# Kernel optimization log

Measured on AMD Instinct MI355X. Metric: run time of the kernel, lower is better.

Reference implementation:

```python
import jax, jax.numpy as jnp
import numpy as np

D_MODEL = 1024
D_FF = 2048
N_EXPERTS = 4
TOP_K = 2
INIT_STD = 0.02


def setup_inputs() -> dict:
    key = jax.random.key(0)
    ks = jax.random.split(key, 5)
    hidden_states = jax.random.normal(ks[0], (2, 2048, D_MODEL), dtype=jnp.float32)
    # gate: nn.Linear(d_model, num_experts, bias=False) -> weight [E, D]
    w_gate = jax.random.normal(ks[1], (N_EXPERTS, D_MODEL), dtype=jnp.float32) * INIT_STD
    # per-expert GLU MLP weights, stacked over the expert axis
    w_gate_proj = jax.random.normal(ks[2], (N_EXPERTS, D_MODEL, D_FF), dtype=jnp.float32) * INIT_STD
    w_up_proj = jax.random.normal(ks[3], (N_EXPERTS, D_MODEL, D_FF), dtype=jnp.float32) * INIT_STD
    w_down_proj = jax.random.normal(ks[4], (N_EXPERTS, D_FF, D_MODEL), dtype=jnp.float32) * INIT_STD
    return {
        "hidden_states": hidden_states,
        "w_gate": w_gate,
        "w_gate_proj": w_gate_proj,
        "w_up_proj": w_up_proj,
        "w_down_proj": w_down_proj,
    }


def reference(hidden_states, w_gate, w_gate_proj, w_up_proj, w_down_proj):
    B, S, D = hidden_states.shape
    x = hidden_states.reshape(-1, D)  # [T, D]
    # --- routing ---
    router_logits = x @ w_gate.T  # [T, E]
    routing_probs = jax.nn.softmax(router_logits.astype(jnp.float32), axis=-1)
    topw, sel = jax.lax.top_k(routing_probs, TOP_K)  # [T, K]
    topw = topw / jnp.sum(topw, axis=-1, keepdims=True)  # norm_topk_prob=True
    topw = topw.astype(x.dtype)
    # combine weights per (token, expert): zero for non-selected experts
    cw = jnp.sum(jax.nn.one_hot(sel, N_EXPERTS, dtype=x.dtype) * topw[..., None], axis=1)  # [T, E]
    # --- expert GLU MLPs (dense over experts, masked combine) ---
    g = jnp.einsum('td,edf->etf', x, w_gate_proj)  # [E, T, F]
    u = jnp.einsum('td,edf->etf', x, w_up_proj)
    h = jax.nn.gelu(g, approximate=False) * u  # torch F.gelu default = exact erf
    y = jnp.einsum('etf,efd->etd', h, w_down_proj)  # [E, T, D]
    out = jnp.einsum('etd,te->td', y, cw)  # weighted scatter-combine
    # dropout p=0.0 (eval) -> identity
    return out.reshape(B, S, D)
```

## Files before the change

kernel.cpp:

```cpp
#include <hip/hip_runtime.h>
#include <hip/hip_bf16.h>
#include <math.h>


typedef float  f32x4 __attribute__((ext_vector_type(4)));
typedef short  s16x8 __attribute__((ext_vector_type(8)));

__device__ __forceinline__ unsigned short f2bf(float f) {
  union { float f; unsigned int u; } v; v.f = f;
  return (unsigned short)((v.u + 0x7fffu + ((v.u >> 16) & 1u)) >> 16);
}

__device__ __forceinline__ void glds16(const void* g, void* l) {
  __builtin_amdgcn_global_load_lds(
      (const __attribute__((address_space(1))) void*)g,
      (__attribute__((address_space(3))) void*)l, 16, 0, 0);
}

__global__ void k_routing(const float* __restrict__ x, const float* __restrict__ wg,
                          float* __restrict__ cw, int* __restrict__ idx,
                          int* __restrict__ cnt) {
  const int lane = threadIdx.x & 63;
  const int tok  = blockIdx.x * 4 + (threadIdx.x >> 6);
  const float* xr = x + (size_t)tok * 1024;
  float a0 = 0.f, a1 = 0.f, a2 = 0.f, a3 = 0.f;
#pragma unroll
  for (int j = 0; j < 16; ++j) {
    const int d = j * 64 + lane;
    const float xv = xr[d];
    a0 += xv * wg[0 * 1024 + d];
    a1 += xv * wg[1 * 1024 + d];
    a2 += xv * wg[2 * 1024 + d];
    a3 += xv * wg[3 * 1024 + d];
  }
#pragma unroll
  for (int off = 32; off; off >>= 1) {
    a0 += __shfl_xor(a0, off);
    a1 += __shfl_xor(a1, off);
    a2 += __shfl_xor(a2, off);
    a3 += __shfl_xor(a3, off);
  }
  if (lane == 0) {
    float l[4] = {a0, a1, a2, a3};
    const float m = fmaxf(fmaxf(l[0], l[1]), fmaxf(l[2], l[3]));
    float p[4];
#pragma unroll
    for (int e = 0; e < 4; ++e) p[e] = expf(l[e] - m);
    int i1 = 0; float b1 = p[0];
#pragma unroll
    for (int e = 1; e < 4; ++e) if (p[e] > b1) { b1 = p[e]; i1 = e; }
    int i2 = -1; float b2 = -1.f;
#pragma unroll
    for (int e = 0; e < 4; ++e) if (e != i1 && p[e] > b2) { b2 = p[e]; i2 = e; }
    const float inv = 1.f / (b1 + b2);
    float o[4] = {0.f, 0.f, 0.f, 0.f};
    o[i1] = b1 * inv; o[i2] = b2 * inv;
    *(float4*)(cw + (size_t)tok * 4) = make_float4(o[0], o[1], o[2], o[3]);
    const int p1 = atomicAdd(&cnt[i1], 1); idx[i1 * 4096 + p1] = tok;
    const int p2 = atomicAdd(&cnt[i2], 1); idx[i2 * 4096 + p2] = tok;
  }
}

__global__ void k_offsets(const int* __restrict__ cnt, int* __restrict__ off) {
  if (threadIdx.x == 0 && blockIdx.x == 0) {
    int o = 0;
#pragma unroll
    for (int e = 0; e < 4; ++e) { off[e] = o; o += (cnt[e] + 127) & ~127; }
  }
}

__global__ void k_cvt_x(const float* __restrict__ in, unsigned short* __restrict__ out) {
  const int i = blockIdx.x * blockDim.x + threadIdx.x;
  const float4 v = ((const float4*)in)[i];
  ushort4 o;
  o.x = f2bf(v.x); o.y = f2bf(v.y); o.z = f2bf(v.z); o.w = f2bf(v.w);
  ((ushort4*)out)[i] = o;
}

__global__ void k_tcvt_all(const float* __restrict__ wgp, const float* __restrict__ wup,
                           const float* __restrict__ wdp,
                           unsigned short* __restrict__ Wgt, unsigned short* __restrict__ Wut,
                           unsigned short* __restrict__ Wdt) {
  __shared__ float t[32][33];
  const int z = blockIdx.z;
  const float* in; unsigned short* out; int R, C, c0, r0;
  if (z < 8) {
    R = 1024; C = 2048;
    const int e = z & 3;
    in  = (z < 4 ? wgp : wup) + (size_t)e * 1024 * 2048;
    out = (z < 4 ? Wgt : Wut) + (size_t)e * 1024 * 2048;
    c0 = blockIdx.x * 32; r0 = blockIdx.y * 32;
  } else {
    R = 2048; C = 1024;
    const int e = z & 3;
    in  = wdp + (size_t)e * 2048 * 1024;
    out = Wdt + (size_t)e * 2048 * 1024;
    c0 = blockIdx.y * 32; r0 = blockIdx.x * 32;
  }
  const int tx = threadIdx.x, ty = threadIdx.y;
#pragma unroll
  for (int i = 0; i < 4; ++i)
    t[ty + 8 * i][tx] = in[(size_t)(r0 + ty + 8 * i) * C + c0 + tx];
  __syncthreads();
#pragma unroll
  for (int i = 0; i < 4; ++i)
    out[(size_t)(c0 + ty + 8 * i) * R + r0 + tx] = f2bf(t[tx][ty + 8 * i]);
}

__global__ __launch_bounds__(256, 2)
void k_gemm1(const unsigned short* __restrict__ Xb,
             const unsigned short* __restrict__ Wgt,
             const unsigned short* __restrict__ Wut,
             unsigned short* __restrict__ H,
             const int* __restrict__ idx, const int* __restrict__ cnt,
             const int* __restrict__ off) {
  const int w  = (blockIdx.x & 7) * 134 + (blockIdx.x >> 3);
  const int bn = w / 67, mt = w % 67;
  const int o1 = off[1] >> 7, o2 = off[2] >> 7, o3 = off[3] >> 7;
  if (mt >= o3 + ((cnt[3] + 127) >> 7)) return;
  const int e  = (mt >= o1) + (mt >= o2) + (mt >= o3);
  const int ob = (e == 0) ? 0 : (e == 1 ? o1 : (e == 2 ? o2 : o3));
  const int cn = cnt[e];
  const int lr0 = (mt - ob) * 128;

  __shared__ __align__(16) unsigned short sA[128 * 64];
  __shared__ __align__(16) unsigned short sG[128 * 64];
  __shared__ __align__(16) unsigned short sU[128 * 64];
  const int tid = threadIdx.x;
  const int lane = tid & 63, wid = tid >> 6;
  const int wm = wid >> 1, wn = wid & 1;

  f32x4 accg[4][4] = {};
  f32x4 accu[4][4] = {};

  const int srow = lane >> 3;
  const int scol = (lane & 7) * 8;
  int tk[4];
#pragma unroll
  for (int i = 0; i < 4; ++i) {
    const int row = (wid * 4 + i) * 8 + srow;
    tk[i] = idx[e * 4096 + min(lr0 + row, cn - 1)];
  }
  const unsigned short* Wg = Wgt + (size_t)e * 2048 * 1024 + (size_t)(bn * 128) * 1024;
  const unsigned short* Wu = Wut + (size_t)e * 2048 * 1024 + (size_t)(bn * 128) * 1024;

  for (int kt = 0; kt < 16; ++kt) {
    const int k0 = kt * 64;
#pragma unroll
    for (int i = 0; i < 4; ++i) {
      const int c = wid * 4 + i;
      const int row = c * 8 + srow;
      glds16(Xb + (size_t)tk[i] * 1024 + k0 + scol, &sA[c * 512]);
      glds16(Wg + (size_t)row * 1024 + k0 + scol, &sG[c * 512]);
      glds16(Wu + (size_t)row * 1024 + k0 + scol, &sU[c * 512]);
    }
    __syncthreads();
#pragma unroll
    for (int ks = 0; ks < 2; ++ks) {
      const int ko = ks * 32 + (lane >> 4) * 8;
      s16x8 a[4], bg[4], bu[4];
#pragma unroll
      for (int mi = 0; mi < 4; ++mi)
        a[mi] = *(const s16x8*)&sA[(wm * 64 + mi * 16 + (lane & 15)) * 64 + ko];
#pragma unroll
      for (int ni = 0; ni < 4; ++ni) {
        bg[ni] = *(const s16x8*)&sG[(wn * 64 + ni * 16 + (lane & 15)) * 64 + ko];
        bu[ni] = *(const s16x8*)&sU[(wn * 64 + ni * 16 + (lane & 15)) * 64 + ko];
      }
#pragma unroll
      for (int mi = 0; mi < 4; ++mi)
#pragma unroll
        for (int ni = 0; ni < 4; ++ni) {
          accg[mi][ni] = __builtin_amdgcn_mfma_f32_16x16x32_bf16(a[mi], bg[ni], accg[mi][ni], 0, 0, 0);
          accu[mi][ni] = __builtin_amdgcn_mfma_f32_16x16x32_bf16(a[mi], bu[ni], accu[mi][ni], 0, 0, 0);
        }
    }
    __syncthreads();
  }
  const int r0 = mt * 128 + wm * 64;
  const int c0 = bn * 128 + wn * 64;
#pragma unroll
  for (int mi = 0; mi < 4; ++mi)
#pragma unroll
    for (int ni = 0; ni < 4; ++ni)
#pragma unroll
      for (int r = 0; r < 4; ++r) {
        const int row = r0 + mi * 16 + (lane >> 4) * 4 + r;
        const int col = c0 + ni * 16 + (lane & 15);
        const float g = accg[mi][ni][r];
        const float u = accu[mi][ni][r];
        const float h = 0.5f * g * (1.0f + erff(g * 0.70710678118654752f)) * u;
        H[(size_t)row * 2048 + col] = f2bf(h);
      }
}

__global__ __launch_bounds__(256, 2)
void k_gemm2(const unsigned short* __restrict__ H,
             const unsigned short* __restrict__ Wdt,
             const float* __restrict__ cw,
             const int* __restrict__ idx, const int* __restrict__ cnt,
             const int* __restrict__ off,
             float* __restrict__ out) {
  const int w  = (blockIdx.x & 7) * 67 + (blockIdx.x >> 3);
  const int mt = w >> 3, bn = w & 7;
  const int o1 = off[1] >> 7, o2 = off[2] >> 7, o3 = off[3] >> 7;
  if (mt >= o3 + ((cnt[3] + 127) >> 7)) return;
  const int e  = (mt >= o1) + (mt >= o2) + (mt >= o3);
  const int ob = (e == 0) ? 0 : (e == 1 ? o1 : (e == 2 ? o2 : o3));
  const int cn = cnt[e];
  const int lr0 = (mt - ob) * 128;

  __shared__ __align__(16) unsigned short sA[128 * 64];
  __shared__ __align__(16) unsigned short sB[128 * 64];
  const int tid = threadIdx.x;
  const int lane = tid & 63, wid = tid >> 6;
  const int wm = wid >> 1, wn = wid & 1;

  f32x4 acc[4][4] = {};
  const int srow = lane >> 3;
  const int scol = (lane & 7) * 8;
  const unsigned short* Ha = H + (size_t)(mt * 128) * 2048;
  const unsigned short* Wd = Wdt + (size_t)e * 1024 * 2048 + (size_t)(bn * 128) * 2048;

  for (int kt = 0; kt < 32; ++kt) {
    const int k0 = kt * 64;
#pragma unroll
    for (int i = 0; i < 4; ++i) {
      const int c = wid * 4 + i;
      const int row = c * 8 + srow;
      glds16(Ha + (size_t)row * 2048 + k0 + scol, &sA[c * 512]);
      glds16(Wd + (size_t)row * 2048 + k0 + scol, &sB[c * 512]);
    }
    __syncthreads();
#pragma unroll
    for (int ks = 0; ks < 2; ++ks) {
      const int ko = ks * 32 + (lane >> 4) * 8;
      s16x8 a[4], b[4];
#pragma unroll
      for (int mi = 0; mi < 4; ++mi)
        a[mi] = *(const s16x8*)&sA[(wm * 64 + mi * 16 + (lane & 15)) * 64 + ko];
#pragma unroll
      for (int ni = 0; ni < 4; ++ni)
        b[ni] = *(const s16x8*)&sB[(wn * 64 + ni * 16 + (lane & 15)) * 64 + ko];
#pragma unroll
      for (int mi = 0; mi < 4; ++mi)
#pragma unroll
        for (int ni = 0; ni < 4; ++ni)
          acc[mi][ni] = __builtin_amdgcn_mfma_f32_16x16x32_bf16(a[mi], b[ni], acc[mi][ni], 0, 0, 0);
    }
    __syncthreads();
  }
#pragma unroll
  for (int mi = 0; mi < 4; ++mi)
#pragma unroll
    for (int r = 0; r < 4; ++r) {
      const int lr = lr0 + wm * 64 + mi * 16 + (lane >> 4) * 4 + r;
      if (lr < cn) {
        const int tok = idx[e * 4096 + lr];
        const float wgt = cw[(size_t)tok * 4 + e];
        float* orow = out + (size_t)tok * 1024 + bn * 128 + wn * 64 + (lane & 15);
#pragma unroll
        for (int ni = 0; ni < 4; ++ni)
          atomicAdd(orow + ni * 16, acc[mi][ni][r] * wgt);
      }
    }
}

extern "C" void kernel_launch(void* const* d_in, const int* in_sizes, int n_in,
                              void* d_out, int out_size, void* d_ws, size_t ws_size,
                              hipStream_t stream) {
  const float* x     = (const float*)d_in[0];
  const float* wgate = (const float*)d_in[1];
  const float* wgp   = (const float*)d_in[2];
  const float* wup   = (const float*)d_in[3];
  const float* wdp   = (const float*)d_in[4];
  float* out = (float*)d_out;

  char* ws = (char*)d_ws;
  float* cw           = (float*)ws;
  int*   idx          = (int*)(ws + 65536);
  int*   cnt          = (int*)(ws + 131072);
  int*   off          = (int*)(ws + 131328);
  unsigned short* Xb  = (unsigned short*)(ws + 131584);
  unsigned short* Wgt = Xb  + (size_t)4096 * 1024;
  unsigned short* Wut = Wgt + (size_t)4 * 2048 * 1024;
  unsigned short* Wdt = Wut + (size_t)4 * 2048 * 1024;
  unsigned short* H   = Wdt + (size_t)4 * 1024 * 2048;

  hipMemsetAsync(cnt, 0, 16, stream);
  hipMemsetAsync(out, 0, (size_t)4096 * 1024 * 4, stream);
  k_routing<<<1024, 256, 0, stream>>>(x, wgate, cw, idx, cnt);
  k_offsets<<<1, 64, 0, stream>>>(cnt, off);
  k_cvt_x<<<4096, 256, 0, stream>>>(x, Xb);
  k_tcvt_all<<<dim3(64, 32, 12), dim3(32, 8), 0, stream>>>(wgp, wup, wdp, Wgt, Wut, Wdt);

  k_gemm1<<<1072, 256, 0, stream>>>(Xb, Wgt, Wut, H, idx, cnt, off);
  k_gemm2<<<536, 256, 0, stream>>>(H, Wdt, cw, idx, cnt, off, out);
}
```

Measured before the change: 327.9 us.

## Double-buffer LDS, interleave gate/up weights, enlarge tiles to 256 rows with 8 waves

Gate and up projection weights are interleaved into one concatenated transposed buffer, so gemm1 loads a single B tile whose alternating 16-column blocks hold g and u. Both GEMMs move to 512-thread blocks with larger tiles (256x128 for gemm1, 128x256 for gemm2) and double-buffered LDS. Prefetch of the next K slice is issued between MFMA phases, with s_setprio raising priority around the MFMA bursts. An XOR swizzle on LDS offsets is meant to reduce bank conflicts. The intent is to hide global-load latency and improve operand reuse. In exchange, the larger tiles pad each expert's token count to 256 rows, wasting more work, and give fewer blocks per launch.

```diff
diff --git a/kernel.cpp b/kernel.cpp
--- a/kernel.cpp
+++ b/kernel.cpp
@@ -16,6 +16,8 @@
       (const __attribute__((address_space(1))) void*)g,
       (__attribute__((address_space(3))) void*)l, 16, 0, 0);
 }
+
+__device__ __forceinline__ int swz(int o) { return o ^ (((o >> 9) & 1) << 5); }
 
 __global__ void k_routing(const float* __restrict__ x, const float* __restrict__ wg,
                           float* __restrict__ cw, int* __restrict__ idx,
@@ -63,9 +65,15 @@
 
 __global__ void k_offsets(const int* __restrict__ cnt, int* __restrict__ off) {
   if (threadIdx.x == 0 && blockIdx.x == 0) {
-    int o = 0;
-#pragma unroll
-    for (int e = 0; e < 4; ++e) { off[e] = o; o += (cnt[e] + 127) & ~127; }
+    int o = 0, q = 0, p = 0;
+#pragma unroll
+    for (int e = 0; e < 4; ++e) {
+      off[e] = o; off[4 + e] = q; off[9 + e] = p;
+      o += (cnt[e] + 255) & ~255;
+      q += (cnt[e] + 255) >> 8;
+      p += (cnt[e] + 127) >> 7;
+    }
+    off[8] = q; off[13] = p;
   }
 }
 
@@ -79,177 +87,269 @@
 
 __global__ void k_tcvt_all(const float* __restrict__ wgp, const float* __restrict__ wup,
                            const float* __restrict__ wdp,
-                           unsigned short* __restrict__ Wgt, unsigned short* __restrict__ Wut,
+                           unsigned short* __restrict__ Wcat,
                            unsigned short* __restrict__ Wdt) {
-  __shared__ float t[32][33];
+  __shared__ float t[64][65];
   const int z = blockIdx.z;
-  const float* in; unsigned short* out; int R, C, c0, r0;
+  const int tx = threadIdx.x, ty = threadIdx.y;
+  const float* in; unsigned short* outp; int R, C, c0, r0, cat = 0, addup = 0;
   if (z < 8) {
     R = 1024; C = 2048;
     const int e = z & 3;
-    in  = (z < 4 ? wgp : wup) + (size_t)e * 1024 * 2048;
-    out = (z < 4 ? Wgt : Wut) + (size_t)e * 1024 * 2048;
-    c0 = blockIdx.x * 32; r0 = blockIdx.y * 32;
+    in   = (z < 4 ? wgp : wup) + (size_t)e * 1024 * 2048;
+    outp = Wcat + (size_t)e * 4096 * 1024;
+    c0 = blockIdx.x * 64; r0 = blockIdx.y * 64;
+    cat = 1; addup = (z >= 4) ? 16 : 0;
   } else {
     R = 2048; C = 1024;
     const int e = z & 3;
-    in  = wdp + (size_t)e * 2048 * 1024;
-    out = Wdt + (size_t)e * 2048 * 1024;
-    c0 = blockIdx.y * 32; r0 = blockIdx.x * 32;
-  }
-  const int tx = threadIdx.x, ty = threadIdx.y;
-#pragma unroll
-  for (int i = 0; i < 4; ++i)
-    t[ty + 8 * i][tx] = in[(size_t)(r0 + ty + 8 * i) * C + c0 + tx];
+    in   = wdp + (size_t)e * 2048 * 1024;
+    outp = Wdt + (size_t)e * 2048 * 1024;
+    c0 = blockIdx.y * 64; r0 = blockIdx.x * 64;
+  }
+#pragma unroll
+  for (int i = 0; i < 16; ++i) {
+    const int r = i * 4 + ty;
+    t[r][tx] = in[(size_t)(r0 + r) * C + c0 + tx];
+  }
   __syncthreads();
 #pragma unroll
-  for (int i = 0; i < 4; ++i)
-    out[(size_t)(c0 + ty + 8 * i) * R + r0 + tx] = f2bf(t[tx][ty + 8 * i]);
-}
-
-__global__ __launch_bounds__(256, 2)
+  for (int i = 0; i < 16; ++i) {
+    const int cc = i * 4 + ty;
+    const int f = c0 + cc;
+    const int orow = cat ? (((f >> 4) << 5) + (f & 15) + addup) : f;
+    outp[(size_t)orow * R + r0 + tx] = f2bf(t[tx][cc]);
+  }
+}
+
+__global__ __launch_bounds__(512, 2)
 void k_gemm1(const unsigned short* __restrict__ Xb,
-             const unsigned short* __restrict__ Wgt,
-             const unsigned short* __restrict__ Wut,
+             const unsigned short* __restrict__ Wcat,
              unsigned short* __restrict__ H,
              const int* __restrict__ idx, const int* __restrict__ cnt,
              const int* __restrict__ off) {
-  const int w  = (blockIdx.x & 7) * 134 + (blockIdx.x >> 3);
-  const int bn = w / 67, mt = w % 67;
-  const int o1 = off[1] >> 7, o2 = off[2] >> 7, o3 = off[3] >> 7;
-  if (mt >= o3 + ((cnt[3] + 127) >> 7)) return;
-  const int e  = (mt >= o1) + (mt >= o2) + (mt >= o3);
-  const int ob = (e == 0) ? 0 : (e == 1 ? o1 : (e == 2 ? o2 : o3));
+  const int w0 = (blockIdx.x & 7) * 72 + (blockIdx.x >> 3);
+  const int bn = w0 / 36, mt = w0 % 36;
+  const int* t1 = off + 4;
+  if (mt >= t1[4]) return;
+  const int e = (mt >= t1[1]) + (mt >= t1[2]) + (mt >= t1[3]);
+  const int local = mt - t1[e];
   const int cn = cnt[e];
-  const int lr0 = (mt - ob) * 128;
-
-  __shared__ __align__(16) unsigned short sA[128 * 64];
-  __shared__ __align__(16) unsigned short sG[128 * 64];
-  __shared__ __align__(16) unsigned short sU[128 * 64];
+  const int lr0 = local * 256;
+  const int hrow0 = off[e] + lr0;
+
+  __shared__ __align__(16) unsigned short lds[2][2][256 * 64];
+
   const int tid = threadIdx.x;
-  const int lane = tid & 63, wid = tid >> 6;
-  const int wm = wid >> 1, wn = wid & 1;
-
-  f32x4 accg[4][4] = {};
-  f32x4 accu[4][4] = {};
-
-  const int srow = lane >> 3;
-  const int scol = (lane & 7) * 8;
+  const int lane = tid & 63, wv = tid >> 6;
+  const int wm = wv >> 2, wn = wv & 3;
+  const int l2 = lane ^ ((lane & 32) >> 4);
+  const int rsub = lane >> 3;
+  const int gk = (l2 & 7) * 8;
+
   int tk[4];
 #pragma unroll
   for (int i = 0; i < 4; ++i) {
-    const int row = (wid * 4 + i) * 8 + srow;
-    tk[i] = idx[e * 4096 + min(lr0 + row, cn - 1)];
-  }
-  const unsigned short* Wg = Wgt + (size_t)e * 2048 * 1024 + (size_t)(bn * 128) * 1024;
-  const unsigned short* Wu = Wut + (size_t)e * 2048 * 1024 + (size_t)(bn * 128) * 1024;
+    const int r = (wv * 4 + i) * 8 + rsub;
+    tk[i] = idx[e * 4096 + min(lr0 + r, max(cn - 1, 0))];
+  }
+  const unsigned short* Wb = Wcat + (size_t)e * 4096 * 1024 + (size_t)(bn * 256) * 1024;
+
+  f32x4 acc[8][4] = {};
+
+#pragma unroll
+  for (int i = 0; i < 4; ++i) {
+    const int c = wv * 4 + i;
+    glds16(Xb + (size_t)tk[i] * 1024 + gk, &lds[0][0][c * 512]);
+    glds16(Wb + (size_t)(c * 8 + rsub) * 1024 + gk, &lds[0][1][c * 512]);
+  }
+  asm volatile("s_waitcnt vmcnt(0)\ns_barrier" ::: "memory");
 
   for (int kt = 0; kt < 16; ++kt) {
-    const int k0 = kt * 64;
-#pragma unroll
-    for (int i = 0; i < 4; ++i) {
-      const int c = wid * 4 + i;
-      const int row = c * 8 + srow;
-      glds16(Xb + (size_t)tk[i] * 1024 + k0 + scol, &sA[c * 512]);
-      glds16(Wg + (size_t)row * 1024 + k0 + scol, &sG[c * 512]);
-      glds16(Wu + (size_t)row * 1024 + k0 + scol, &sU[c * 512]);
+    const int cur = kt & 1;
+    const unsigned short* Abuf = lds[cur][0];
+    const unsigned short* Bbuf = lds[cur][1];
+    unsigned short* An = lds[cur ^ 1][0];
+    unsigned short* Bn = lds[cur ^ 1][1];
+    const int kn = (kt + 1) * 64;
+    const bool pf = (kt < 15);
+
+    s16x8 bfr[4][2];
+#pragma unroll
+    for (int p = 0; p < 4; ++p) {
+      s16x8 afr[2][2];
+#pragma unroll
+      for (int j = 0; j < 2; ++j) {
+        const int row = wm * 128 + (p * 2 + j) * 16 + (lane & 15);
+#pragma unroll
+        for (int ks = 0; ks < 2; ++ks) {
+          const int o = swz((row * 64 + ks * 32 + (lane >> 4) * 8) * 2);
+          afr[j][ks] = *(const s16x8*)((const char*)Abuf + o);
+        }
+      }
+      if (p == 0) {
+#pragma unroll
+        for (int ni = 0; ni < 4; ++ni) {
+          const int row = wn * 64 + ni * 16 + (lane & 15);
+#pragma unroll
+          for (int ks = 0; ks < 2; ++ks) {
+            const int o = swz((row * 64 + ks * 32 + (lane >> 4) * 8) * 2);
+            bfr[ni][ks] = *(const s16x8*)((const char*)Bbuf + o);
+          }
+        }
+        if (pf) {
+#pragma unroll
+          for (int i = 0; i < 4; ++i) {
+            const int c = wv * 4 + i;
+            glds16(Xb + (size_t)tk[i] * 1024 + kn + gk, &An[c * 512]);
+          }
+        }
+      }
+      if (p == 1 && pf) {
+#pragma unroll
+        for (int i = 0; i < 4; ++i) {
+          const int c = wv * 4 + i;
+          glds16(Wb + (size_t)(c * 8 + rsub) * 1024 + kn + gk, &Bn[c * 512]);
+        }
+      }
+      asm volatile("s_barrier" ::: "memory");
+      __builtin_amdgcn_s_setprio(1);
+#pragma unroll
+      for (int j = 0; j < 2; ++j) {
+        const int mi = p * 2 + j;
+#pragma unroll
+        for (int ni = 0; ni < 4; ++ni) {
+          acc[mi][ni] = __builtin_amdgcn_mfma_f32_16x16x32_bf16(afr[j][0], bfr[ni][0], acc[mi][ni], 0, 0, 0);
+          acc[mi][ni] = __builtin_amdgcn_mfma_f32_16x16x32_bf16(afr[j][1], bfr[ni][1], acc[mi][ni], 0, 0, 0);
+        }
+      }
+      __builtin_amdgcn_s_setprio(0);
+      if (p < 3) { asm volatile("s_barrier" ::: "memory"); }
+      else       { asm volatile("s_waitcnt vmcnt(0)\ns_barrier" ::: "memory"); }
     }
-    __syncthreads();
-#pragma unroll
-    for (int ks = 0; ks < 2; ++ks) {
-      const int ko = ks * 32 + (lane >> 4) * 8;
-      s16x8 a[4], bg[4], bu[4];
-#pragma unroll
-      for (int mi = 0; mi < 4; ++mi)
-        a[mi] = *(const s16x8*)&sA[(wm * 64 + mi * 16 + (lane & 15)) * 64 + ko];
-#pragma unroll
-      for (int ni = 0; ni < 4; ++ni) {
-        bg[ni] = *(const s16x8*)&sG[(wn * 64 + ni * 16 + (lane & 15)) * 64 + ko];
-        bu[ni] = *(const s16x8*)&sU[(wn * 64 + ni * 16 + (lane & 15)) * 64 + ko];
-      }
-#pragma unroll
-      for (int mi = 0; mi < 4; ++mi)
-#pragma unroll
-        for (int ni = 0; ni < 4; ++ni) {
-          accg[mi][ni] = __builtin_amdgcn_mfma_f32_16x16x32_bf16(a[mi], bg[ni], accg[mi][ni], 0, 0, 0);
-          accu[mi][ni] = __builtin_amdgcn_mfma_f32_16x16x32_bf16(a[mi], bu[ni], accu[mi][ni], 0, 0, 0);
-        }
-    }
-    __syncthreads();
-  }
-  const int r0 = mt * 128 + wm * 64;
-  const int c0 = bn * 128 + wn * 64;
-#pragma unroll
-  for (int mi = 0; mi < 4; ++mi)
-#pragma unroll
-    for (int ni = 0; ni < 4; ++ni)
+  }
+
+  const int rbase = hrow0 + wm * 128;
+#pragma unroll
+  for (int mi = 0; mi < 8; ++mi)
+#pragma unroll
+    for (int q = 0; q < 2; ++q)
 #pragma unroll
       for (int r = 0; r < 4; ++r) {
-        const int row = r0 + mi * 16 + (lane >> 4) * 4 + r;
-        const int col = c0 + ni * 16 + (lane & 15);
-        const float g = accg[mi][ni][r];
-        const float u = accu[mi][ni][r];
+        const int row = rbase + mi * 16 + (lane >> 4) * 4 + r;
+        const int col = bn * 128 + wn * 32 + q * 16 + (lane & 15);
+        const float g = acc[mi][2 * q][r];
+        const float u = acc[mi][2 * q + 1][r];
         const float h = 0.5f * g * (1.0f + erff(g * 0.70710678118654752f)) * u;
         H[(size_t)row * 2048 + col] = f2bf(h);
       }
 }
 
-__global__ __launch_bounds__(256, 2)
+__global__ __launch_bounds__(512, 2)
 void k_gemm2(const unsigned short* __restrict__ H,
              const unsigned short* __restrict__ Wdt,
              const float* __restrict__ cw,
              const int* __restrict__ idx, const int* __restrict__ cnt,
-             const int* __restrict__ off,
-             float* __restrict__ out) {
-  const int w  = (blockIdx.x & 7) * 67 + (blockIdx.x >> 3);
-  const int mt = w >> 3, bn = w & 7;
-  const int o1 = off[1] >> 7, o2 = off[2] >> 7, o3 = off[3] >> 7;
-  if (mt >= o3 + ((cnt[3] + 127) >> 7)) return;
-  const int e  = (mt >= o1) + (mt >= o2) + (mt >= o3);
-  const int ob = (e == 0) ? 0 : (e == 1 ? o1 : (e == 2 ? o2 : o3));
+             const int* __restrict__ off, float* __restrict__ out) {
+  const int w0 = (blockIdx.x & 7) * 34 + (blockIdx.x >> 3);
+  const int mt = w0 >> 2, bn = w0 & 3;
+  const int* t2 = off + 9;
+  if (mt >= t2[4]) return;
+  const int e = (mt >= t2[1]) + (mt >= t2[2]) + (mt >= t2[3]);
+  const int local = mt - t2[e];
   const int cn = cnt[e];
-  const int lr0 = (mt - ob) * 128;
-
-  __shared__ __align__(16) unsigned short sA[128 * 64];
-  __shared__ __align__(16) unsigned short sB[128 * 64];
+  const int lr0 = local * 128;
+  const int hrow0 = off[e] + lr0;
+
+  __shared__ __align__(16) unsigned short lds[2][(128 + 256) * 64];
+
   const int tid = threadIdx.x;
-  const int lane = tid & 63, wid = tid >> 6;
-  const int wm = wid >> 1, wn = wid & 1;
+  const int lane = tid & 63, wv = tid >> 6;
+  const int wm = wv >> 2, wn = wv & 3;
+  const int l2 = lane ^ ((lane & 32) >> 4);
+  const int rsub = lane >> 3;
+  const int gk = (l2 & 7) * 8;
+
+  const unsigned short* Ha = H + (size_t)hrow0 * 2048;
+  const unsigned short* Wd = Wdt + (size_t)e * 1024 * 2048 + (size_t)(bn * 256) * 2048;
 
   f32x4 acc[4][4] = {};
-  const int srow = lane >> 3;
-  const int scol = (lane & 7) * 8;
-  const unsigned short* Ha = H + (size_t)(mt * 128) * 2048;
-  const unsigned short* Wd = Wdt + (size_t)e * 1024 * 2048 + (size_t)(bn * 128) * 2048;
+
+#pragma unroll
+  for (int i = 0; i < 2; ++i) {
+    const int c = wv * 2 + i;
+    glds16(Ha + (size_t)(c * 8 + rsub) * 2048 + gk, &lds[0][c * 512]);
+  }
+#pragma unroll
+  for (int i = 0; i < 4; ++i) {
+    const int c = wv * 4 + i;
+    glds16(Wd + (size_t)(c * 8 + rsub) * 2048 + gk, &lds[0][128 * 64 + c * 512]);
+  }
+  asm volatile("s_waitcnt vmcnt(0)\ns_barrier" ::: "memory");
 
   for (int kt = 0; kt < 32; ++kt) {
-    const int k0 = kt * 64;
-#pragma unroll
-    for (int i = 0; i < 4; ++i) {
-      const int c = wid * 4 + i;
-      const int row = c * 8 + srow;
-      glds16(Ha + (size_t)row * 2048 + k0 + scol, &sA[c * 512]);
-      glds16(Wd + (size_t)row * 2048 + k0 + scol, &sB[c * 512]);
+    const int cur = kt & 1;
+    const unsigned short* Abuf = &lds[cur][0];
+    const unsigned short* Bbuf = &lds[cur][128 * 64];
+    unsigned short* An = &lds[cur ^ 1][0];
+    unsigned short* Bn = &lds[cur ^ 1][128 * 64];
+    const int kn = (kt + 1) * 64;
+    const bool pf = (kt < 31);
+
+    s16x8 bfr[4][2];
+#pragma unroll
+    for (int p = 0; p < 2; ++p) {
+      s16x8 afr[2][2];
+#pragma unroll
+      for (int j = 0; j < 2; ++j) {
+        const int row = wm * 64 + (p * 2 + j) * 16 + (lane & 15);
+#pragma unroll
+        for (int ks = 0; ks < 2; ++ks) {
+          const int o = swz((row * 64 + ks * 32 + (lane >> 4) * 8) * 2);
+          afr[j][ks] = *(const s16x8*)((const char*)Abuf + o);
+        }
+      }
+      if (p == 0) {
+#pragma unroll
+        for (int ni = 0; ni < 4; ++ni) {
+          const int row = wn * 64 + ni * 16 + (lane & 15);
+#pragma unroll
+          for (int ks = 0; ks < 2; ++ks) {
+            const int o = swz((row * 64 + ks * 32 + (lane >> 4) * 8) * 2);
+            bfr[ni][ks] = *(const s16x8*)((const char*)Bbuf + o);
+          }
+        }
+        if (pf) {
+#pragma unroll
+          for (int i = 0; i < 4; ++i) {
+            const int c = wv * 4 + i;
+            glds16(Wd + (size_t)(c * 8 + rsub) * 2048 + kn + gk, &Bn[c * 512]);
+          }
+        }
+      } else if (pf) {
+#pragma unroll
+        for (int i = 0; i < 2; ++i) {
+          const int c = wv * 2 + i;
+          glds16(Ha + (size_t)(c * 8 + rsub) * 2048 + kn + gk, &An[c * 512]);
+        }
+      }
+      asm volatile("s_barrier" ::: "memory");
+      __builtin_amdgcn_s_setprio(1);
+#pragma unroll
+      for (int j = 0; j < 2; ++j) {
+        const int mi = p * 2 + j;
+#pragma unroll
+        for (int ni = 0; ni < 4; ++ni) {
+          acc[mi][ni] = __builtin_amdgcn_mfma_f32_16x16x32_bf16(afr[j][0], bfr[ni][0], acc[mi][ni], 0, 0, 0);
+          acc[mi][ni] = __builtin_amdgcn_mfma_f32_16x16x32_bf16(afr[j][1], bfr[ni][1], acc[mi][ni], 0, 0, 0);
+        }
+      }
+      __builtin_amdgcn_s_setprio(0);
+      if (p == 0) { asm volatile("s_barrier" ::: "memory"); }
+      else        { asm volatile("s_waitcnt vmcnt(0)\ns_barrier" ::: "memory"); }
     }
-    __syncthreads();
-#pragma unroll
-    for (int ks = 0; ks < 2; ++ks) {
-      const int ko = ks * 32 + (lane >> 4) * 8;
-      s16x8 a[4], b[4];
-#pragma unroll
-      for (int mi = 0; mi < 4; ++mi)
-        a[mi] = *(const s16x8*)&sA[(wm * 64 + mi * 16 + (lane & 15)) * 64 + ko];
-#pragma unroll
-      for (int ni = 0; ni < 4; ++ni)
-        b[ni] = *(const s16x8*)&sB[(wn * 64 + ni * 16 + (lane & 15)) * 64 + ko];
-#pragma unroll
-      for (int mi = 0; mi < 4; ++mi)
-#pragma unroll
-        for (int ni = 0; ni < 4; ++ni)
-          acc[mi][ni] = __builtin_amdgcn_mfma_f32_16x16x32_bf16(a[mi], b[ni], acc[mi][ni], 0, 0, 0);
-    }
-    __syncthreads();
-  }
+  }
+
 #pragma unroll
   for (int mi = 0; mi < 4; ++mi)
 #pragma unroll
@@ -258,7 +358,7 @@
       if (lr < cn) {
         const int tok = idx[e * 4096 + lr];
         const float wgt = cw[(size_t)tok * 4 + e];
-        float* orow = out + (size_t)tok * 1024 + bn * 128 + wn * 64 + (lane & 15);
+        float* orow = out + (size_t)tok * 1024 + bn * 256 + wn * 64 + (lane & 15);
 #pragma unroll
         for (int ni = 0; ni < 4; ++ni)
           atomicAdd(orow + ni * 16, acc[mi][ni][r] * wgt);
@@ -277,23 +377,22 @@
   float* out = (float*)d_out;
 
   char* ws = (char*)d_ws;
-  float* cw           = (float*)ws;
-  int*   idx          = (int*)(ws + 65536);
-  int*   cnt          = (int*)(ws + 131072);
-  int*   off          = (int*)(ws + 131328);
-  unsigned short* Xb  = (unsigned short*)(ws + 131584);
-  unsigned short* Wgt = Xb  + (size_t)4096 * 1024;
-  unsigned short* Wut = Wgt + (size_t)4 * 2048 * 1024;
-  unsigned short* Wdt = Wut + (size_t)4 * 2048 * 1024;
-  unsigned short* H   = Wdt + (size_t)4 * 1024 * 2048;
+  float* cw            = (float*)ws;
+  int*   idx           = (int*)(ws + 65536);
+  int*   cnt           = (int*)(ws + 131072);
+  int*   off           = (int*)(ws + 131136);
+  unsigned short* Xb   = (unsigned short*)(ws + 131584);
+  unsigned short* Wcat = Xb   + (size_t)4096 * 1024;
+  unsigned short* Wdt  = Wcat + (size_t)4 * 4096 * 1024;
+  unsigned short* H    = Wdt  + (size_t)4 * 1024 * 2048;
 
   hipMemsetAsync(cnt, 0, 16, stream);
   hipMemsetAsync(out, 0, (size_t)4096 * 1024 * 4, stream);
   k_routing<<<1024, 256, 0, stream>>>(x, wgate, cw, idx, cnt);
   k_offsets<<<1, 64, 0, stream>>>(cnt, off);
   k_cvt_x<<<4096, 256, 0, stream>>>(x, Xb);
-  k_tcvt_all<<<dim3(64, 32, 12), dim3(32, 8), 0, stream>>>(wgp, wup, wdp, Wgt, Wut, Wdt);
-
-  k_gemm1<<<1072, 256, 0, stream>>>(Xb, Wgt, Wut, H, idx, cnt, off);
-  k_gemm2<<<536, 256, 0, stream>>>(H, Wdt, cw, idx, cnt, off, out);
-}
+  k_tcvt_all<<<dim3(32, 16, 12), dim3(64, 4), 0, stream>>>(wgp, wup, wdp, Wcat, Wdt);
+
+  k_gemm1<<<576, 512, 0, stream>>>(Xb, Wcat, H, idx, cnt, off);
+  k_gemm2<<<272, 512, 0, stream>>>(H, Wdt, cw, idx, cnt, off, out);
+}
```

Result: slower. 363.9 us (+11.0%).
